# Kernel tuning notes

Measured on AMD Instinct MI355X. Metric: run time of the kernel, lower is better.

The kernel has to match this reference:

```python
import jax, jax.numpy as jnp
import numpy as np

D_MODEL = 512
NUM_HEADS = 8
HEAD_DIM = D_MODEL // NUM_HEADS


def setup_inputs() -> dict:
    key = jax.random.key(0)
    ks = jax.random.split(key, 11)
    N, S, D = 2, 4096, D_MODEL
    s = 1.0 / np.sqrt(D)
    return {
        "query": jax.random.normal(ks[0], (N, S, D), jnp.float32),
        "key": jax.random.normal(ks[1], (N, S, D), jnp.float32),
        "value": jax.random.normal(ks[2], (N, S, D), jnp.float32),
        "Wq": jax.random.normal(ks[3], (D, D), jnp.float32) * s,
        "bq": jnp.zeros((D,), jnp.float32),
        "Wk": jax.random.normal(ks[4], (D, D), jnp.float32) * s,
        "bk": jnp.zeros((D,), jnp.float32),
        "Wv": jax.random.normal(ks[5], (D, D), jnp.float32) * s,
        "bv": jnp.zeros((D,), jnp.float32),
        "Wo": jax.random.normal(ks[6], (D, D), jnp.float32) * s,
        "bo": jnp.zeros((D,), jnp.float32),
    }


def reference(query, key, value, Wq, bq, Wk, bk, Wv, bv, Wo, bo):
    N, S, D = query.shape
    H, Hd = NUM_HEADS, HEAD_DIM
    # Linear projections (torch Linear: x @ W.T + b), split heads -> [N,H,S,Hd]
    Q = (query @ Wq.T + bq).reshape(N, S, H, Hd).transpose(0, 2, 1, 3)
    K = (key @ Wk.T + bk).reshape(N, S, H, Hd).transpose(0, 2, 1, 3)
    V = (value @ Wv.T + bv).reshape(N, S, H, Hd).transpose(0, 2, 1, 3)
    scale = 1.0 / np.sqrt(Hd)
    energy = jnp.einsum("nhqd,nhkd->nhqk", Q, K) * scale  # [N,H,S,S]
    attention = jax.nn.softmax(energy, axis=-1)
    out = jnp.einsum("nhqk,nhkd->nhqd", attention, V)
    out = out.transpose(0, 2, 1, 3).reshape(N, S, D)
    return out @ Wo.T + bo
```

## Files before the change

kernel.cpp:

```cpp
#include <hip/hip_runtime.h>


#define SEQ 4096
#define PERHEAD 262144
#define CEXPF 0.18033688011112042f

typedef short bf16x8 __attribute__((ext_vector_type(8)));
typedef short bf16x4 __attribute__((ext_vector_type(4)));
typedef float f32x4 __attribute__((ext_vector_type(4)));
typedef unsigned short u16;
typedef unsigned int u32;

__device__ inline float bf2f(u16 h) {
    return __uint_as_float(((u32)h) << 16);
}
__device__ inline u16 f2bf(float f) {
    u32 u = __float_as_uint(f);
    u = (u + 0x7fffu + ((u >> 16) & 1u)) >> 16;
    return (u16)u;
}
__device__ inline u32 packtrunc(float lo, float hi) {
    return __builtin_amdgcn_perm(__float_as_uint(hi), __float_as_uint(lo),
                                 0x07060302u);
}
__device__ inline uint4 pack8(float4 a, float4 b) {
    uint4 r;
    r.x = (u32)f2bf(a.x) | ((u32)f2bf(a.y) << 16);
    r.y = (u32)f2bf(a.z) | ((u32)f2bf(a.w) << 16);
    r.z = (u32)f2bf(b.x) | ((u32)f2bf(b.y) << 16);
    r.w = (u32)f2bf(b.z) | ((u32)f2bf(b.w) << 16);
    return r;
}

__global__ void detect_dtype(const u16* __restrict__ W, int* __restrict__ flag) {
    const int lane = threadIdx.x & 63;
    u16 u = W[2 * lane];
    int e = (u >> 7) & 0xFF;
    int plaus = (u == 0) || (e >= 100 && e <= 132);
    unsigned long long m = __ballot(plaus);
    if (lane == 0) *flag = (__popcll(m) >= 48) ? 0 : 1;
}

__global__ __launch_bounds__(256) void prep(
    const void* __restrict__ W0, const void* __restrict__ W1,
    const void* __restrict__ W2, const void* __restrict__ W3,
    const void* __restrict__ b0, const void* __restrict__ b1,
    const void* __restrict__ b2, const void* __restrict__ b3,
    u16* __restrict__ Wc, u16* __restrict__ bc, const int* __restrict__ flag)
{
    const int m = blockIdx.y;
    const void* Ws = (m == 0) ? W0 : (m == 1) ? W1 : (m == 2) ? W2 : W3;
    const void* bs = (m == 0) ? b0 : (m == 1) ? b1 : (m == 2) ? b2 : b3;
    const int isf32 = *flag;
    if (blockIdx.x < 128) {
        const int idx = blockIdx.x * 2048 + threadIdx.x * 8;
        u16* dst = Wc + (size_t)m * 262144 + idx;
        if (isf32) {
            const float4* s = (const float4*)((const float*)Ws + idx);
            *(uint4*)dst = pack8(s[0], s[1]);
        } else {
            *(uint4*)dst = *(const uint4*)((const u16*)Ws + idx);
        }
    } else if (threadIdx.x < 64) {
        const int idx = threadIdx.x * 8;
        u16* dst = bc + m * 512 + idx;
        if (isf32) {
            const float4* s = (const float4*)((const float*)bs + idx);
            *(uint4*)dst = pack8(s[0], s[1]);
        } else {
            *(uint4*)dst = *(const uint4*)((const u16*)bs + idx);
        }
    }
}

template <int A_BF16>
__device__ inline void gemm_body(
    const void* __restrict__ Av, const u16* __restrict__ B,
    const u16* __restrict__ bias, void* __restrict__ outv,
    int isf32, int mode, float scale, int m0, int n0,
    u16* As, u16* Bs)
{
    const int tid = threadIdx.x;
    const int wave = tid >> 6, lane = tid & 63, quad = lane >> 4, ln = lane & 15;
    const int qr = wave >> 1, qc = wave & 1;

    f32x4 acc[4][4];
#pragma unroll
    for (int i = 0; i < 4; i++)
#pragma unroll
        for (int j = 0; j < 4; j++) acc[i][j] = (f32x4){0.f, 0.f, 0.f, 0.f};

    const int srow = tid >> 1;
    const int scol = (tid & 1) * 16;
    const uint4*  Ag16 = (const uint4*) ((const u16*)Av + (size_t)(m0 + srow) * 512 + scol);
    const float4* Ag32 = (const float4*)((const float*)Av + (size_t)(m0 + srow) * 512 + scol);
    const uint4*  Bg   = (const uint4*) (B + (size_t)(n0 + srow) * 512 + scol);
    uint4* Al = (uint4*)(As + srow * 40 + scol);
    uint4* Bl = (uint4*)(Bs + srow * 40 + scol);

    for (int kk = 0; kk < 512; kk += 32) {
        __syncthreads();
        uint4 aw0, aw1;
        if (A_BF16 || !isf32) {
            aw0 = Ag16[0]; aw1 = Ag16[1];
            Ag16 += 4;
        } else {
            float4 f0 = Ag32[0], f1 = Ag32[1], f2 = Ag32[2], f3 = Ag32[3];
            Ag32 += 8;
            aw0 = pack8(f0, f1); aw1 = pack8(f2, f3);
        }
        uint4 bw0 = Bg[0], bw1 = Bg[1];
        Bg += 4;
        Al[0] = aw0; Al[1] = aw1; Bl[0] = bw0; Bl[1] = bw1;
        __syncthreads();
        bf16x8 af[4], bfr[4];
#pragma unroll
        for (int mi = 0; mi < 4; mi++)
            af[mi] = *(const bf16x8*)(As + (qr * 64 + mi * 16 + ln) * 40 + quad * 8);
#pragma unroll
        for (int ni = 0; ni < 4; ni++)
            bfr[ni] = *(const bf16x8*)(Bs + (qc * 64 + ni * 16 + ln) * 40 + quad * 8);
#pragma unroll
        for (int mi = 0; mi < 4; mi++)
#pragma unroll
            for (int ni = 0; ni < 4; ni++)
                acc[mi][ni] = __builtin_amdgcn_mfma_f32_16x16x32_bf16(
                    af[mi], bfr[ni], acc[mi][ni], 0, 0, 0);
    }

#pragma unroll
    for (int ni = 0; ni < 4; ni++) {
        const int col = n0 + qc * 64 + ni * 16 + ln;
        const float bvv = bf2f(bias[col]);
#pragma unroll
        for (int mi = 0; mi < 4; mi++) {
#pragma unroll
            for (int r = 0; r < 4; r++) {
                const int row = m0 + qr * 64 + mi * 16 + quad * 4 + r;
                const float v = (acc[mi][ni][r] + bvv) * scale;
                if (mode == 0) {
                    const size_t idx = (size_t)row * 512 + col;
                    if (isf32) ((float*)outv)[idx] = v;
                    else       ((u16*)outv)[idx] = f2bf(v);
                } else {
                    const int b = row >> 12, s = row & 4095;
                    const int h = col >> 6, hd = col & 63;
                    size_t idx;
                    if (mode == 1)
                        idx = (size_t)(b * 8 + h) * PERHEAD + (size_t)s * 64 + hd;
                    else
                        idx = (size_t)(b * 8 + h) * PERHEAD + (size_t)hd * 4096 + s;
                    ((u16*)outv)[idx] = f2bf(v);
                }
            }
        }
    }
}

__global__ __launch_bounds__(256) void qkv_proj(
    const void* __restrict__ q, const void* __restrict__ k, const void* __restrict__ v,
    const u16* __restrict__ Wc, const u16* __restrict__ bc,
    u16* __restrict__ Qh, u16* __restrict__ Kh, u16* __restrict__ Vt,
    const int* __restrict__ flag)
{
    __shared__ __align__(16) u16 As[128 * 40];
    __shared__ __align__(16) u16 Bs[128 * 40];
    const int z = blockIdx.z;
    const void* Av = (z == 0) ? q : (z == 1) ? k : v;
    void* outv = (z == 0) ? (void*)Qh : (z == 1) ? (void*)Kh : (void*)Vt;
    const int mode = (z == 2) ? 2 : 1;
    const float scale = (z == 0) ? CEXPF : 1.0f;
    gemm_body<0>(Av, Wc + (size_t)z * 262144, bc + z * 512, outv,
                 *flag, mode, scale, blockIdx.y * 128, blockIdx.x * 128, As, Bs);
}

__global__ __launch_bounds__(256) void out_proj(
    const void* __restrict__ Av, const u16* __restrict__ Wc,
    const u16* __restrict__ bc, void* __restrict__ outv,
    const int* __restrict__ flag)
{
    __shared__ __align__(16) u16 As[128 * 40];
    __shared__ __align__(16) u16 Bs[128 * 40];
    gemm_body<1>(Av, Wc + (size_t)3 * 262144, bc + 3 * 512, outv,
                 *flag, 0, 1.0f, blockIdx.y * 128, blockIdx.x * 128, As, Bs);
}

__global__ __launch_bounds__(256) void attn_kernel(
    const u16* __restrict__ Q, const u16* __restrict__ K,
    const u16* __restrict__ Vt, u16* __restrict__ AO)
{
    __shared__ __align__(16) u16 Ks[64 * 72];
    __shared__ __align__(16) u16 Vs[64 * 72];

    const int tid = threadIdx.x;
    const int w = tid >> 6, lane = tid & 63, quad = lane >> 4, ln = lane & 15;
    const int bh = blockIdx.y;
    const int q0 = blockIdx.x * 128;
    const size_t base = (size_t)bh * PERHEAD;

    bf16x8 qf[2][2];
#pragma unroll
    for (int qt = 0; qt < 2; qt++) {
        const uint4* qp = (const uint4*)(Q + base + (size_t)(q0 + w * 32 + qt * 16 + ln) * 64);
        uint4 v0 = qp[quad], v1 = qp[4 + quad];
        qf[qt][0] = *(bf16x8*)&v0;
        qf[qt][1] = *(bf16x8*)&v1;
    }

    bf16x8 ones;
#pragma unroll
    for (int j = 0; j < 8; j++) ones[j] = (short)0x3F80;

    f32x4 oT[2][4];
    f32x4 lacc[2];
#pragma unroll
    for (int qt = 0; qt < 2; qt++) {
        lacc[qt] = (f32x4){0.f, 0.f, 0.f, 0.f};
#pragma unroll
        for (int mt = 0; mt < 4; mt++) oT[qt][mt] = (f32x4){0.f, 0.f, 0.f, 0.f};
    }

    const int srow = tid >> 2;
    const int sc = (tid & 3) * 16;
    const uint4* Kg = (const uint4*)(K + base + (size_t)srow * 64 + sc);
    const uint4* Vg = (const uint4*)(Vt + base + (size_t)srow * 4096 + sc);
    uint4* Kl = (uint4*)(Ks + srow * 72 + sc);
    uint4* Vl = (uint4*)(Vs + srow * 72 + sc);

    for (int k0 = 0; k0 < SEQ; k0 += 64) {
        __syncthreads();
        {
            uint4 a = Kg[0], b = Kg[1], c = Vg[0], d = Vg[1];
            Kg += 512;
            Vg += 8;
            Kl[0] = a; Kl[1] = b; Vl[0] = c; Vl[1] = d;
        }
        __syncthreads();

        f32x4 s[2][4];
#pragma unroll
        for (int t = 0; t < 2; t++)
#pragma unroll
            for (int kt = 0; kt < 4; kt++) {
                bf16x8 kf = *(const bf16x8*)(Ks + (kt * 16 + ln) * 72 + t * 32 + quad * 8);
#pragma unroll
                for (int qt = 0; qt < 2; qt++) {
                    if (t == 0)
                        s[qt][kt] = __builtin_amdgcn_mfma_f32_16x16x32_bf16(
                            kf, qf[qt][0], (f32x4){0.f, 0.f, 0.f, 0.f}, 0, 0, 0);
                    else
                        s[qt][kt] = __builtin_amdgcn_mfma_f32_16x16x32_bf16(
                            kf, qf[qt][1], s[qt][kt], 0, 0, 0);
                }
            }

        bf16x8 pf[2][2];
#pragma unroll
        for (int qt = 0; qt < 2; qt++)
#pragma unroll
            for (int c = 0; c < 2; c++) {
                float e0 = exp2f(s[qt][2 * c][0]), e1 = exp2f(s[qt][2 * c][1]);
                float e2 = exp2f(s[qt][2 * c][2]), e3 = exp2f(s[qt][2 * c][3]);
                float f0 = exp2f(s[qt][2 * c + 1][0]), f1 = exp2f(s[qt][2 * c + 1][1]);
                float f2 = exp2f(s[qt][2 * c + 1][2]), f3 = exp2f(s[qt][2 * c + 1][3]);
                u32 w0 = packtrunc(e0, e1), w1 = packtrunc(e2, e3);
                u32 w2 = packtrunc(f0, f1), w3 = packtrunc(f2, f3);
                uint4 pk = {w0, w1, w2, w3};
                pf[qt][c] = *(bf16x8*)&pk;
            }

#pragma unroll
        for (int qt = 0; qt < 2; qt++)
#pragma unroll
            for (int c = 0; c < 2; c++)
                lacc[qt] = __builtin_amdgcn_mfma_f32_16x16x32_bf16(
                    ones, pf[qt][c], lacc[qt], 0, 0, 0);

#pragma unroll
        for (int c = 0; c < 2; c++)
#pragma unroll
            for (int mt = 0; mt < 4; mt++) {
                const u16* vrow = Vs + (mt * 16 + ln) * 72 + c * 32 + quad * 4;
                bf16x4 v0 = *(const bf16x4*)(vrow);
                bf16x4 v1 = *(const bf16x4*)(vrow + 16);
                bf16x8 vf;
#pragma unroll
                for (int j = 0; j < 4; j++) { vf[j] = v0[j]; vf[4 + j] = v1[j]; }
#pragma unroll
                for (int qt = 0; qt < 2; qt++)
                    oT[qt][mt] = __builtin_amdgcn_mfma_f32_16x16x32_bf16(
                        vf, pf[qt][c], oT[qt][mt], 0, 0, 0);
            }
    }

    const int b = bh >> 3, h = bh & 7;
#pragma unroll
    for (int qt = 0; qt < 2; qt++) {
        const float inv = 1.0f / lacc[qt][0];
        const int qrow = q0 + w * 32 + qt * 16 + ln;
        u16* op = AO + (size_t)(b * 4096 + qrow) * 512 + h * 64 + quad * 4;
#pragma unroll
        for (int mt = 0; mt < 4; mt++) {
            uint2 pk;
            pk.x = (u32)f2bf(oT[qt][mt][0] * inv) | ((u32)f2bf(oT[qt][mt][1] * inv) << 16);
            pk.y = (u32)f2bf(oT[qt][mt][2] * inv) | ((u32)f2bf(oT[qt][mt][3] * inv) << 16);
            *(uint2*)(op + mt * 16) = pk;
        }
    }
}

extern "C" void kernel_launch(void* const* d_in, const int* in_sizes, int n_in,
                              void* d_out, int out_size, void* d_ws, size_t ws_size,
                              hipStream_t stream)
{
    (void)in_sizes; (void)n_in; (void)out_size; (void)ws_size;
    const void* q  = d_in[0];
    const void* k  = d_in[1];
    const void* v  = d_in[2];
    const void* Wq = d_in[3];
    const void* bq = d_in[4];
    const void* Wk = d_in[5];
    const void* bk = d_in[6];
    const void* Wv = d_in[7];
    const void* bv = d_in[8];
    const void* Wo = d_in[9];
    const void* bo = d_in[10];

    u16* ws = (u16*)d_ws;
    u16* Kh = ws;
    u16* Vt = ws + 4194304;
    u16* AO = ws + 8388608;
    u16* Wc = ws + 12582912;
    u16* bc = ws + 12582912 + 1048576;
    int* flag = (int*)(ws + 12582912 + 1048576 + 2048);
    u16* Qh = (u16*)d_out;

    detect_dtype<<<1, 64, 0, stream>>>((const u16*)Wq, flag);
    prep<<<dim3(129, 4), 256, 0, stream>>>(Wq, Wk, Wv, Wo, bq, bk, bv, bo,
                                           Wc, bc, flag);
    qkv_proj<<<dim3(4, 64, 3), 256, 0, stream>>>(q, k, v, Wc, bc, Qh, Kh, Vt, flag);
    attn_kernel<<<dim3(32, 16), 256, 0, stream>>>(Qh, Kh, Vt, AO);
    out_proj<<<dim3(4, 64), 256, 0, stream>>>(AO, Wc, bc, d_out, flag);
}
```

Measured before the change: 283.4 us.

## Widen GEMM K-tile, permute V layout, shrink attention blocks with XCD mapping

The projection GEMMs now stage 64-wide K tiles, issuing global loads before the barrier, which halves the number of syncs per tile. V is written in a permuted sequence order so the attention kernel can read each V fragment with a single 16-byte LDS load instead of two 8-byte loads and a shuffle. The attention kernel moves to 128-thread blocks covering 64 queries, launched as a 1D grid of 1024 blocks mapped so each XCD handles two heads, which is meant to improve L2 reuse of K/V and occupancy. exp2f is replaced by raw v_exp_f32, dropping denormal and range handling. The risks are more LDS per GEMM block and more K/V reloads per query across the smaller attention blocks.

```diff
diff --git a/kernel.cpp b/kernel.cpp
--- a/kernel.cpp
+++ b/kernel.cpp
@@ -6,7 +6,6 @@
 #define CEXPF 0.18033688011112042f
 
 typedef short bf16x8 __attribute__((ext_vector_type(8)));
-typedef short bf16x4 __attribute__((ext_vector_type(4)));
 typedef float f32x4 __attribute__((ext_vector_type(4)));
 typedef unsigned short u16;
 typedef unsigned int u32;
@@ -18,6 +17,11 @@
     u32 u = __float_as_uint(f);
     u = (u + 0x7fffu + ((u >> 16) & 1u)) >> 16;
     return (u16)u;
+}
+__device__ inline float exp2_raw(float x) {
+    float r;
+    asm("v_exp_f32 %0, %1" : "=v"(r) : "v"(x));
+    return r;
 }
 __device__ inline u32 packtrunc(float lo, float hi) {
     return __builtin_amdgcn_perm(__float_as_uint(hi), __float_as_uint(lo),
@@ -91,41 +95,50 @@
         for (int j = 0; j < 4; j++) acc[i][j] = (f32x4){0.f, 0.f, 0.f, 0.f};
 
     const int srow = tid >> 1;
-    const int scol = (tid & 1) * 16;
-    const uint4*  Ag16 = (const uint4*) ((const u16*)Av + (size_t)(m0 + srow) * 512 + scol);
-    const float4* Ag32 = (const float4*)((const float*)Av + (size_t)(m0 + srow) * 512 + scol);
-    const uint4*  Bg   = (const uint4*) (B + (size_t)(n0 + srow) * 512 + scol);
-    uint4* Al = (uint4*)(As + srow * 40 + scol);
-    uint4* Bl = (uint4*)(Bs + srow * 40 + scol);
-
-    for (int kk = 0; kk < 512; kk += 32) {
+    const int sc = (tid & 1) * 32;
+    const uint4*  Ag16 = (const uint4*) ((const u16*)Av + (size_t)(m0 + srow) * 512 + sc);
+    const float4* Ag32 = (const float4*)((const float*)Av + (size_t)(m0 + srow) * 512 + sc);
+    const uint4*  Bg   = (const uint4*) (B + (size_t)(n0 + srow) * 512 + sc);
+    uint4* Al = (uint4*)(As + srow * 72 + sc);
+    uint4* Bl = (uint4*)(Bs + srow * 72 + sc);
+
+    for (int kk = 0; kk < 512; kk += 64) {
+        uint4 aw[4], bw[4];
+        if (A_BF16 || !isf32) {
+#pragma unroll
+            for (int i = 0; i < 4; i++) aw[i] = Ag16[i];
+            Ag16 += 8;
+        } else {
+            float4 f[8];
+#pragma unroll
+            for (int i = 0; i < 8; i++) f[i] = Ag32[i];
+            Ag32 += 16;
+            aw[0] = pack8(f[0], f[1]); aw[1] = pack8(f[2], f[3]);
+            aw[2] = pack8(f[4], f[5]); aw[3] = pack8(f[6], f[7]);
+        }
+#pragma unroll
+        for (int i = 0; i < 4; i++) bw[i] = Bg[i];
+        Bg += 8;
         __syncthreads();
-        uint4 aw0, aw1;
-        if (A_BF16 || !isf32) {
-            aw0 = Ag16[0]; aw1 = Ag16[1];
-            Ag16 += 4;
-        } else {
-            float4 f0 = Ag32[0], f1 = Ag32[1], f2 = Ag32[2], f3 = Ag32[3];
-            Ag32 += 8;
-            aw0 = pack8(f0, f1); aw1 = pack8(f2, f3);
-        }
-        uint4 bw0 = Bg[0], bw1 = Bg[1];
-        Bg += 4;
-        Al[0] = aw0; Al[1] = aw1; Bl[0] = bw0; Bl[1] = bw1;
+#pragma unroll
+        for (int i = 0; i < 4; i++) { Al[i] = aw[i]; Bl[i] = bw[i]; }
         __syncthreads();
-        bf16x8 af[4], bfr[4];
-#pragma unroll
-        for (int mi = 0; mi < 4; mi++)
-            af[mi] = *(const bf16x8*)(As + (qr * 64 + mi * 16 + ln) * 40 + quad * 8);
-#pragma unroll
-        for (int ni = 0; ni < 4; ni++)
-            bfr[ni] = *(const bf16x8*)(Bs + (qc * 64 + ni * 16 + ln) * 40 + quad * 8);
-#pragma unroll
-        for (int mi = 0; mi < 4; mi++)
+#pragma unroll
+        for (int t2 = 0; t2 < 2; t2++) {
+            bf16x8 af[4], bfr[4];
+#pragma unroll
+            for (int mi = 0; mi < 4; mi++)
+                af[mi] = *(const bf16x8*)(As + (qr * 64 + mi * 16 + ln) * 72 + t2 * 32 + quad * 8);
 #pragma unroll
             for (int ni = 0; ni < 4; ni++)
-                acc[mi][ni] = __builtin_amdgcn_mfma_f32_16x16x32_bf16(
-                    af[mi], bfr[ni], acc[mi][ni], 0, 0, 0);
+                bfr[ni] = *(const bf16x8*)(Bs + (qc * 64 + ni * 16 + ln) * 72 + t2 * 32 + quad * 8);
+#pragma unroll
+            for (int mi = 0; mi < 4; mi++)
+#pragma unroll
+                for (int ni = 0; ni < 4; ni++)
+                    acc[mi][ni] = __builtin_amdgcn_mfma_f32_16x16x32_bf16(
+                        af[mi], bfr[ni], acc[mi][ni], 0, 0, 0);
+        }
     }
 
 #pragma unroll
@@ -146,10 +159,13 @@
                     const int b = row >> 12, s = row & 4095;
                     const int h = col >> 6, hd = col & 63;
                     size_t idx;
-                    if (mode == 1)
+                    if (mode == 1) {
                         idx = (size_t)(b * 8 + h) * PERHEAD + (size_t)s * 64 + hd;
-                    else
-                        idx = (size_t)(b * 8 + h) * PERHEAD + (size_t)hd * 4096 + s;
+                    } else {
+                        const int sp = (s & ~63) | (s & 32) | ((s & 12) << 1)
+                                     | ((s & 16) >> 2) | (s & 3);
+                        idx = (size_t)(b * 8 + h) * PERHEAD + (size_t)hd * 4096 + sp;
+                    }
                     ((u16*)outv)[idx] = f2bf(v);
                 }
             }
@@ -163,8 +179,8 @@
     u16* __restrict__ Qh, u16* __restrict__ Kh, u16* __restrict__ Vt,
     const int* __restrict__ flag)
 {
-    __shared__ __align__(16) u16 As[128 * 40];
-    __shared__ __align__(16) u16 Bs[128 * 40];
+    __shared__ __align__(16) u16 As[128 * 72];
+    __shared__ __align__(16) u16 Bs[128 * 72];
     const int z = blockIdx.z;
     const void* Av = (z == 0) ? q : (z == 1) ? k : v;
     void* outv = (z == 0) ? (void*)Qh : (z == 1) ? (void*)Kh : (void*)Vt;
@@ -179,13 +195,13 @@
     const u16* __restrict__ bc, void* __restrict__ outv,
     const int* __restrict__ flag)
 {
-    __shared__ __align__(16) u16 As[128 * 40];
-    __shared__ __align__(16) u16 Bs[128 * 40];
+    __shared__ __align__(16) u16 As[128 * 72];
+    __shared__ __align__(16) u16 Bs[128 * 72];
     gemm_body<1>(Av, Wc + (size_t)3 * 262144, bc + 3 * 512, outv,
                  *flag, 0, 1.0f, blockIdx.y * 128, blockIdx.x * 128, As, Bs);
 }
 
-__global__ __launch_bounds__(256) void attn_kernel(
+__global__ __launch_bounds__(128) void attn_kernel(
     const u16* __restrict__ Q, const u16* __restrict__ K,
     const u16* __restrict__ Vt, u16* __restrict__ AO)
 {
@@ -194,8 +210,9 @@
 
     const int tid = threadIdx.x;
     const int w = tid >> 6, lane = tid & 63, quad = lane >> 4, ln = lane & 15;
-    const int bh = blockIdx.y;
-    const int q0 = blockIdx.x * 128;
+    const int xcd = blockIdx.x & 7, sub = blockIdx.x >> 3;
+    const int bh = xcd * 2 + (sub >> 6);
+    const int q0 = (sub & 63) * 64;
     const size_t base = (size_t)bh * PERHEAD;
 
     bf16x8 qf[2][2];
@@ -220,21 +237,21 @@
         for (int mt = 0; mt < 4; mt++) oT[qt][mt] = (f32x4){0.f, 0.f, 0.f, 0.f};
     }
 
-    const int srow = tid >> 2;
-    const int sc = (tid & 3) * 16;
+    const int srow = tid >> 1;
+    const int sc = (tid & 1) * 32;
     const uint4* Kg = (const uint4*)(K + base + (size_t)srow * 64 + sc);
     const uint4* Vg = (const uint4*)(Vt + base + (size_t)srow * 4096 + sc);
     uint4* Kl = (uint4*)(Ks + srow * 72 + sc);
     uint4* Vl = (uint4*)(Vs + srow * 72 + sc);
 
     for (int k0 = 0; k0 < SEQ; k0 += 64) {
+        uint4 kw0 = Kg[0], kw1 = Kg[1], kw2 = Kg[2], kw3 = Kg[3];
+        uint4 vw0 = Vg[0], vw1 = Vg[1], vw2 = Vg[2], vw3 = Vg[3];
+        Kg += 512;
+        Vg += 8;
         __syncthreads();
-        {
-            uint4 a = Kg[0], b = Kg[1], c = Vg[0], d = Vg[1];
-            Kg += 512;
-            Vg += 8;
-            Kl[0] = a; Kl[1] = b; Vl[0] = c; Vl[1] = d;
-        }
+        Kl[0] = kw0; Kl[1] = kw1; Kl[2] = kw2; Kl[3] = kw3;
+        Vl[0] = vw0; Vl[1] = vw1; Vl[2] = vw2; Vl[3] = vw3;
         __syncthreads();
 
         f32x4 s[2][4];
@@ -259,10 +276,10 @@
         for (int qt = 0; qt < 2; qt++)
 #pragma unroll
             for (int c = 0; c < 2; c++) {
-                float e0 = exp2f(s[qt][2 * c][0]), e1 = exp2f(s[qt][2 * c][1]);
-                float e2 = exp2f(s[qt][2 * c][2]), e3 = exp2f(s[qt][2 * c][3]);
-                float f0 = exp2f(s[qt][2 * c + 1][0]), f1 = exp2f(s[qt][2 * c + 1][1]);
-                float f2 = exp2f(s[qt][2 * c + 1][2]), f3 = exp2f(s[qt][2 * c + 1][3]);
+                float e0 = exp2_raw(s[qt][2 * c][0]), e1 = exp2_raw(s[qt][2 * c][1]);
+                float e2 = exp2_raw(s[qt][2 * c][2]), e3 = exp2_raw(s[qt][2 * c][3]);
+                float f0 = exp2_raw(s[qt][2 * c + 1][0]), f1 = exp2_raw(s[qt][2 * c + 1][1]);
+                float f2 = exp2_raw(s[qt][2 * c + 1][2]), f3 = exp2_raw(s[qt][2 * c + 1][3]);
                 u32 w0 = packtrunc(e0, e1), w1 = packtrunc(e2, e3);
                 u32 w2 = packtrunc(f0, f1), w3 = packtrunc(f2, f3);
                 uint4 pk = {w0, w1, w2, w3};
@@ -280,12 +297,7 @@
         for (int c = 0; c < 2; c++)
 #pragma unroll
             for (int mt = 0; mt < 4; mt++) {
-                const u16* vrow = Vs + (mt * 16 + ln) * 72 + c * 32 + quad * 4;
-                bf16x4 v0 = *(const bf16x4*)(vrow);
-                bf16x4 v1 = *(const bf16x4*)(vrow + 16);
-                bf16x8 vf;
-#pragma unroll
-                for (int j = 0; j < 4; j++) { vf[j] = v0[j]; vf[4 + j] = v1[j]; }
+                bf16x8 vf = *(const bf16x8*)(Vs + (mt * 16 + ln) * 72 + c * 32 + quad * 8);
 #pragma unroll
                 for (int qt = 0; qt < 2; qt++)
                     oT[qt][mt] = __builtin_amdgcn_mfma_f32_16x16x32_bf16(
@@ -339,6 +351,6 @@
     prep<<<dim3(129, 4), 256, 0, stream>>>(Wq, Wk, Wv, Wo, bq, bk, bv, bo,
                                            Wc, bc, flag);
     qkv_proj<<<dim3(4, 64, 3), 256, 0, stream>>>(q, k, v, Wc, bc, Qh, Kh, Vt, flag);
-    attn_kernel<<<dim3(32, 16), 256, 0, stream>>>(Qh, Kh, Vt, AO);
+    attn_kernel<<<1024, 128, 0, stream>>>(Qh, Kh, Vt, AO);
     out_proj<<<dim3(4, 64), 256, 0, stream>>>(AO, Wc, bc, d_out, flag);
 }
```

New measurement: 309.9 us. 1.09x slower.
